# Optimization experiments

Hardware: AMD Instinct MI355X
Metric: run time of the kernel (lower is better)

Reference implementation:

```python
import jax, jax.numpy as jnp
import numpy as np

CONF_THRES = 0.1
IOU_THRES = 0.6
MAX_DET = 300
MAX_WH = 4096.0  # class offset for non-agnostic NMS
NEG_SLOPE = 0.01  # nn.LeakyReLU default


def xywh2xyxy(p):
    xy, wh = p[..., :2], p[..., 2:4]
    return jnp.concatenate([xy - wh / 2, xy + wh / 2], axis=-1)


def pairwise_iou(a, b):
    area_a = (a[:, 2] - a[:, 0]) * (a[:, 3] - a[:, 1])
    area_b = (b[:, 2] - b[:, 0]) * (b[:, 3] - b[:, 1])
    lt = jnp.maximum(a[:, None, :2], b[None, :, :2])
    rb = jnp.minimum(a[:, None, 2:], b[None, :, 2:])
    wh = jnp.clip(rb - lt, 0.0)
    inter = wh[..., 0] * wh[..., 1]
    return inter / (area_a[:, None] + area_b[None, :] - inter + 1e-7)


def nms_single(pred):  # pred: [N, 5+nc]
    boxes = xywh2xyxy(pred[:, :4])
    scores = pred[:, 5:] * pred[:, 4:5]  # obj * cls
    conf = jnp.max(scores, axis=1)
    cls = jnp.argmax(scores, axis=1)
    conf = jnp.where(conf > CONF_THRES, conf, 0.0)
    topv, topi = jax.lax.top_k(conf, MAX_DET)
    b = boxes[topi]                      # [K,4]
    c = cls[topi]
    valid = topv > CONF_THRES
    bo = b + (c.astype(b.dtype) * MAX_WH)[:, None]  # class-offset boxes
    iou = pairwise_iou(bo, bo)           # [K,K]
    idx = jnp.arange(MAX_DET)
    def body(i, keep):
        sup = keep[i] & (iou[i] > IOU_THRES) & (idx > i)
        return keep & ~sup
    keep = jax.lax.fori_loop(0, MAX_DET, body, valid)
    return b, keep


def bilinear_sample(feat, y, x):  # feat [C,H,W], y/x [K,P] -> [C,K,P]
    C, H, W = feat.shape
    y = jnp.clip(y, 0.0, H - 1.0)
    x = jnp.clip(x, 0.0, W - 1.0)
    y0 = jnp.floor(y).astype(jnp.int32)
    x0 = jnp.floor(x).astype(jnp.int32)
    y1 = jnp.minimum(y0 + 1, H - 1)
    x1 = jnp.minimum(x0 + 1, W - 1)
    ly = y - y0
    lx = x - x0
    return (feat[:, y0, x0] * ((1 - ly) * (1 - lx))
            + feat[:, y0, x1] * ((1 - ly) * lx)
            + feat[:, y1, x0] * (ly * (1 - lx))
            + feat[:, y1, x1] * (ly * lx))


def roi_align_1x1(feat, boxes, scale):  # feat [C,H,W], boxes [K,4] xyxy (input-px)
    b = boxes * scale
    w = jnp.maximum(b[:, 2] - b[:, 0], 1.0)
    h = jnp.maximum(b[:, 3] - b[:, 1], 1.0)
    off = jnp.array([0.5, 1.5], dtype=boxes.dtype)
    xs = b[:, 0:1] + off[None, :] * (w[:, None] / 2.0)  # [K,2]
    ys = b[:, 1:2] + off[None, :] * (h[:, None] / 2.0)
    yy = ys[:, jnp.array([0, 0, 1, 1])]  # [K,4] 2x2 grid
    xx = xs[:, jnp.array([0, 1, 0, 1])]
    v = bilinear_sample(feat, yy, xx)    # [C,K,4]
    return jnp.mean(v, axis=2).T         # [K,C]


def rescale_boxes(bbox, hw, hw0):  # scale_coords + normalize by orig shape
    gain = jnp.minimum(hw[0] / hw0[0], hw[1] / hw0[1])
    pad_x = (hw[1] - hw0[1] * gain) / 2.0
    pad_y = (hw[0] - hw0[0] * gain) / 2.0
    x1 = jnp.clip((bbox[:, 0] - pad_x) / gain, 0.0, hw0[1])
    y1 = jnp.clip((bbox[:, 1] - pad_y) / gain, 0.0, hw0[0])
    x2 = jnp.clip((bbox[:, 2] - pad_x) / gain, 0.0, hw0[1])
    y2 = jnp.clip((bbox[:, 3] - pad_y) / gain, 0.0, hw0[0])
    # divide by shapes[i][0] indexed [w,h,w,h]
    return jnp.stack([x1 / hw0[1], y1 / hw0[0], x2 / hw0[1], y2 / hw0[0]], axis=1)


def setup_inputs() -> dict:
    key = jax.random.key(0)
    ks = jax.random.split(key, 10)
    B, N, NC = 8, 25500, 80
    xy = jax.random.uniform(ks[0], (B, N, 2), minval=0.0, maxval=640.0)
    wh = jax.random.uniform(ks[1], (B, N, 2), minval=8.0, maxval=160.0)
    obj = jax.random.uniform(ks[2], (B, N, 1))
    cls = jax.random.uniform(ks[3], (B, N, NC))
    preds = jnp.concatenate([xy, wh, obj, cls], axis=-1)
    feat1 = jax.random.normal(ks[4], (B, 128, 80, 80), dtype=jnp.float32)
    feat2 = jax.random.normal(ks[5], (B, 256, 40, 40), dtype=jnp.float32)
    feat3 = jax.random.normal(ks[6], (B, 512, 20, 20), dtype=jnp.float32)
    feat4 = jax.random.normal(ks[7], (B, 1024, 10, 10), dtype=jnp.float32)
    orig_hw = jnp.tile(jnp.array([[720.0, 1280.0]], dtype=jnp.float32), (B, 1))
    W1 = jax.random.normal(ks[8], (1920, 256), dtype=jnp.float32) * 0.02
    b1 = jnp.zeros((256,), dtype=jnp.float32)
    W2 = jax.random.normal(ks[9], (256, 256), dtype=jnp.float32) * 0.02
    b2 = jnp.zeros((256,), dtype=jnp.float32)
    return {"preds": preds, "feat1": feat1, "feat2": feat2, "feat3": feat3,
            "feat4": feat4, "orig_hw": orig_hw, "W1": W1, "b1": b1,
            "W2": W2, "b2": b2}


def reference(preds, feat1, feat2, feat3, feat4, orig_hw, W1, b1, W2, b2):
    preds = jax.lax.stop_gradient(preds)  # out.detach() in the original
    hw = jnp.array(feat1.shape[-2:], dtype=preds.dtype) * 8.0  # network input h,w
    boxes, keep = jax.vmap(nms_single)(preds)  # [B,K,4], [B,K]
    f1 = jax.vmap(lambda f, b: roi_align_1x1(f, b, 1.0 / 8))(feat1, boxes)
    f2 = jax.vmap(lambda f, b: roi_align_1x1(f, b, 1.0 / 16))(feat2, boxes)
    f3 = jax.vmap(lambda f, b: roi_align_1x1(f, b, 1.0 / 32))(feat3, boxes)
    f4 = jax.vmap(lambda f, b: roi_align_1x1(f, b, 1.0 / 64))(feat4, boxes)
    f = jnp.concatenate([f1, f2, f3, f4], axis=-1)  # [B,K,1920]
    h = jax.nn.leaky_relu(f @ W1 + b1, NEG_SLOPE)
    h = jax.nn.leaky_relu(h @ W2 + b2, NEG_SLOPE)   # [B,K,256]
    bb = jax.vmap(lambda b, s: rescale_boxes(b, hw, s))(boxes, orig_hw)
    out = jnp.concatenate([bb, h], axis=-1)  # [B,K,260]
    return out * keep[..., None].astype(out.dtype)
```

## Files before the change

kernel.cpp:

```cpp
#include <hip/hip_runtime.h>
#include <hip/hip_bf16.h>
#include <cstdint>
#include <cstddef>

#define NBATCH 8
#define NANCH 25500
#define MAXDET 300
#define NBINS 2048
#define SCAT_BLKS 64

typedef __bf16 bf16x8 __attribute__((ext_vector_type(8)));
typedef float floatx4 __attribute__((ext_vector_type(4)));
typedef unsigned long long ull;

__device__ __forceinline__ int conf_bin(float v) {
  unsigned bits = __float_as_uint(v);
  int bin = (int)((bits - 0x3D800000u) >> 14);
  return bin > (NBINS - 1) ? (NBINS - 1) : bin;
}

#define CONF_TILE 64
__global__ __launch_bounds__(256) void conf_kernel(const float* __restrict__ preds,
                                                   float* __restrict__ conf,
                                                   int* __restrict__ cls,
                                                   int* __restrict__ zmem, int zints,
                                                   int total) {
  if (blockIdx.x < 33) {
    int base = blockIdx.x * 1024;
    #pragma unroll
    for (int k = 0; k < 4; ++k) {
      int i = base + k * 256 + threadIdx.x;
      if (i < zints) zmem[i] = 0;
    }
  }
  __shared__ float s[CONF_TILE * 85];
  int base = blockIdx.x * CONF_TILE;
  int nA = total - base; if (nA > CONF_TILE) nA = CONF_TILE;
  int n4 = (nA * 85) >> 2;
  const float4* g4 = (const float4*)(preds + (size_t)base * 85);
  float4* s4 = (float4*)s;
  for (int i = threadIdx.x; i < n4; i += 256) s4[i] = g4[i];
  __syncthreads();
  int lane16 = threadIdx.x & 15;
  int sub = threadIdx.x >> 4;
  #pragma unroll
  for (int r = 0; r < 4; ++r) {
    int a = r * 16 + sub;
    if (a < nA) {
      const float* row = s + a * 85;
      float obj = row[4];
      float best = -1.0f; int bc = 0;
      #pragma unroll
      for (int j = 0; j < 5; ++j) {
        int c = lane16 * 5 + j;
        float v = row[5 + c] * obj;
        if (v > best) { best = v; bc = c; }
      }
      #pragma unroll
      for (int m = 1; m < 16; m <<= 1) {
        float ov = __shfl_xor(best, m, 64);
        int   oc = __shfl_xor(bc,   m, 64);
        if (ov > best || (ov == best && oc < bc)) { best = ov; bc = oc; }
      }
      if (lane16 == 0) {
        int idx = base + a;
        conf[idx] = (best > 0.1f) ? best : 0.0f;
        cls[idx] = bc;
      }
    }
  }
}

struct TransArgs {
  const float* src[6];
  __hip_bfloat16* dst[6];
  int C[6], HW[6], tx[6], tpb[6], start[6];
};

__global__ __launch_bounds__(256) void trans_scatter_kernel(TransArgs a,
                                                            const float* __restrict__ conf,
                                                            const float* __restrict__ preds,
                                                            const int* __restrict__ clsg,
                                                            int* __restrict__ ghist,
                                                            int* __restrict__ gcnt,
                                                            int* __restrict__ ctr1,
                                                            float* __restrict__ gV,
                                                            int* __restrict__ gI,
                                                            float4* __restrict__ gBox) {
  #pragma clang fp contract(off)
  __shared__ __align__(16) char smem[8448];
  int bid = blockIdx.x;
  int t = threadIdx.y * 32 + threadIdx.x;

  if (bid < SCAT_BLKS) {
    int b = bid >> 3, seg = bid & 7;
    int* s_h = (int*)smem;
    int* shv = (int*)(smem + 8192);
    #pragma unroll
    for (int k = 0; k < 8; ++k) s_h[t + k * 256] = 0;
    if (t == 0) shv[0] = NBINS;
    __syncthreads();
    const int N4 = NANCH >> 2;
    int i0 = (N4 * seg) >> 3, i1 = (N4 * (seg + 1)) >> 3;
    const float4* cf4 = (const float4*)(conf + (size_t)b * NANCH);
    for (int i = i0 + t; i < i1; i += 256) {
      float4 v = cf4[i];
      if (v.x > 0.1f) atomicAdd(&s_h[conf_bin(v.x)], 1);
      if (v.y > 0.1f) atomicAdd(&s_h[conf_bin(v.y)], 1);
      if (v.z > 0.1f) atomicAdd(&s_h[conf_bin(v.z)], 1);
      if (v.w > 0.1f) atomicAdd(&s_h[conf_bin(v.w)], 1);
    }
    __syncthreads();
    #pragma unroll
    for (int k = 0; k < 8; ++k) {
      int bin = t + k * 256;
      int c = s_h[bin];
      if (c) atomicAdd(&ghist[b * NBINS + bin], c);
    }
    __syncthreads();
    if (t == 0) {
      __threadfence();
      atomicAdd(&ctr1[b], 1);
      while (atomicAdd(&ctr1[b], 0) < 8) __builtin_amdgcn_s_sleep(2);
      __threadfence();
    }
    __syncthreads();
    int r[8], suf[8], rs[8];
    int w = t >> 6, lane = t & 63;
    {
      #pragma unroll
      for (int k = 0; k < 8; ++k)
        r[k] = atomicAdd(&ghist[b * NBINS + (w * 8 + k) * 64 + lane], 0);
      int bsum = 0;
      #pragma unroll
      for (int k = 0; k < 8; ++k) {
        int s = r[k];
        #pragma unroll
        for (int d = 1; d < 64; d <<= 1) {
          int o = __shfl_down(s, d, 64);
          if (lane + d < 64) s += o;
        }
        suf[k] = s - r[k];
        rs[k] = __shfl(s, 0, 64);
        bsum += rs[k];
      }
      if (lane == 0) shv[4 + w] = bsum;
    }
    __syncthreads();
    {
      int p1 = shv[5], p2 = shv[6], p3 = shv[7];
      int total = shv[4] + p1 + p2 + p3;
      int target = total < 300 ? total : 300;
      int RS = (w == 0) ? (p1 + p2 + p3) : (w == 1) ? (p2 + p3) : (w == 2) ? p3 : 0;
      int run = RS;
      #pragma unroll
      for (int k = 7; k >= 0; --k) {
        int Sx = run + suf[k] + r[k];
        int Sx1 = Sx - r[k];
        int bin = (w * 8 + k) * 64 + lane;
        s_h[bin] = Sx1;
        if (total > 0 && Sx >= target && Sx1 < target) shv[0] = bin;
        run += rs[k];
      }
    }
    __syncthreads();
    int T = shv[0];
    for (int i = i0 + t; i < i1; i += 256) {
      float4 v4 = cf4[i];
      int ib = i * 4;
      float vv[4] = {v4.x, v4.y, v4.z, v4.w};
      #pragma unroll
      for (int q = 0; q < 4; ++q) {
        float v = vv[q];
        if (v > 0.1f) {
          int bin = conf_bin(v);
          if (bin >= T) {
            int slot = s_h[bin] + atomicAdd(&gcnt[b * NBINS + bin], 1);
            int idx = ib + q;
            const float* p = preds + ((size_t)b * NANCH + idx) * 85;
            float cx = p[0], cy = p[1], wq = p[2], hq = p[3];
            float hw2 = wq * 0.5f, hh2 = hq * 0.5f;
            float x1 = cx - hw2, y1 = cy - hh2, x2 = cx + hw2, y2 = cy + hh2;
            int c = clsg[(size_t)b * NANCH + idx];
            size_t g = (size_t)b * NANCH + slot;
            gV[g] = v;
            gI[g] = idx | (c << 20);
            gBox[g] = make_float4(x1, y1, x2, y2);
          }
        }
      }
    }
    return;
  }

  {
    float (*tile)[33] = (float(*)[33])smem;
    int bid2 = bid - SCAT_BLKS;
    int s = 0;
    #pragma unroll
    for (int i = 1; i < 6; ++i) if (bid2 >= a.start[i]) s = i;
    int local = bid2 - a.start[s];
    int C = a.C[s], HW = a.HW[s], tx0 = a.tx[s], tpb = a.tpb[s];
    int b = local / tpb;
    int rem = local - b * tpb;
    int p0 = (rem % tx0) * 32;
    int c0 = (rem / tx0) * 32;
    const float* inb = a.src[s] + (size_t)b * C * HW;
    __hip_bfloat16* outb = a.dst[s] + (size_t)b * C * HW;
    int tx = threadIdx.x, ty = threadIdx.y;
    #pragma unroll
    for (int k = 0; k < 32; k += 8) {
      int c = c0 + ty + k, p = p0 + tx;
      if (c < C && p < HW) tile[ty + k][tx] = inb[(size_t)c * HW + p];
    }
    __syncthreads();
    #pragma unroll
    for (int k = 0; k < 32; k += 8) {
      int p = p0 + ty + k, c = c0 + tx;
      if (p < HW && c < C) outb[(size_t)p * C + c] = __float2bfloat16(tile[tx][ty + k]);
    }
  }
}

__global__ __launch_bounds__(1024) void nms_kernel(const float* __restrict__ gV,
                                                   const int* __restrict__ gI,
                                                   const float4* __restrict__ gBox,
                                                   const int* __restrict__ ghist,
                                                   float* __restrict__ boxesWs, int* __restrict__ keepWs,
                                                   const float* __restrict__ orig_hw,
                                                   float* __restrict__ out) {
  #pragma clang fp contract(off)
  __shared__ __align__(16) char smem[30208];
  int*    s_h  = (int*)smem;
  float4* bo4  = (float4*)(smem + 8192);
  float (*bxx)[4] = (float(*)[4])(smem + 12992);
  ull   (*mask)[5] = (ull(*)[5])(smem + 17792);
  ull* keepw = (ull*)(smem + 29792);
  ull* nzrow = (ull*)(smem + 29832);
  int* shv   = (int*)(smem + 29872);
  int b = blockIdx.x;
  int t = threadIdx.x;

  if (t < 300) {
    bo4[t] = make_float4(0.0f, 0.0f, 0.0f, 0.0f);
    bxx[t][0] = 0.0f; bxx[t][1] = 0.0f; bxx[t][2] = 0.0f; bxx[t][3] = 0.0f;
  }
  if (t < 5) nzrow[t] = 0ULL;
  if (t == 0) { shv[0] = NBINS; shv[2] = 0; }
  {
    int r[8], suf[8], rs[8];
    int w = t >> 6, lane = t & 63;
    if (t < 256) {
      #pragma unroll
      for (int k = 0; k < 8; ++k)
        r[k] = ghist[b * NBINS + (w * 8 + k) * 64 + lane];
      int bsum = 0;
      #pragma unroll
      for (int k = 0; k < 8; ++k) {
        int s = r[k];
        #pragma unroll
        for (int d = 1; d < 64; d <<= 1) {
          int o = __shfl_down(s, d, 64);
          if (lane + d < 64) s += o;
        }
        suf[k] = s - r[k];
        rs[k] = __shfl(s, 0, 64);
        bsum += rs[k];
      }
      if (lane == 0) shv[4 + w] = bsum;
    }
    __syncthreads();
    if (t < 256) {
      int p1 = shv[5], p2 = shv[6], p3 = shv[7];
      int total = shv[4] + p1 + p2 + p3;
      int target = total < 300 ? total : 300;
      int RS = (w == 0) ? (p1 + p2 + p3) : (w == 1) ? (p2 + p3) : (w == 2) ? p3 : 0;
      int run = RS;
      #pragma unroll
      for (int k = 7; k >= 0; --k) {
        int Sx = run + suf[k] + r[k];
        int Sx1 = Sx - r[k];
        int bin = (w * 8 + k) * 64 + lane;
        s_h[bin] = Sx;
        if (total > 0 && Sx >= target && Sx1 < target) { shv[0] = bin; shv[2] = Sx; }
        run += rs[k];
      }
      if (t == 0) shv[1] = total;
    }
  }
  __syncthreads();
  int total = shv[1];
  int Kslots = shv[2];
  int nvalid = total < 300 ? total : 300;

  if (t >= nvalid && t < 300) {
    size_t bi = ((size_t)(b * 300 + t)) * 4;
    boxesWs[bi + 0] = 0.0f; boxesWs[bi + 1] = 0.0f;
    boxesWs[bi + 2] = 0.0f; boxesWs[bi + 3] = 0.0f;
  }
  if (t < 5) {
    int n = nvalid - t * 64;
    keepw[t] = (n <= 0) ? 0ULL : (n >= 64 ? ~0ULL : ((1ULL << n) - 1ULL));
  }

  {
    const float* vb = gV + (size_t)b * NANCH;
    const int*   ib2 = gI + (size_t)b * NANCH;
    for (int sIdx = t; sIdx < Kslots; sIdx += 1024) {
      float v = vb[sIdx];
      unsigned code = (unsigned)ib2[sIdx];
      int id = (int)(code & 0xFFFFFu);
      int bin = conf_bin(v);
      int lo = (bin + 1 < NBINS) ? s_h[bin + 1] : 0;
      int hi = s_h[bin];
      int rank = lo;
      for (int j = lo; j < hi; ++j) {
        float vj = vb[j];
        int ij = ib2[j] & 0xFFFFF;
        int gt = vj > v;
        int eq = (vj == v) & (ij < id);
        rank += gt | eq;
      }
      if (rank < 300) {
        float4 bx = gBox[(size_t)b * NANCH + sIdx];
        bxx[rank][0] = bx.x; bxx[rank][1] = bx.y; bxx[rank][2] = bx.z; bxx[rank][3] = bx.w;
        size_t bi = ((size_t)(b * 300 + rank)) * 4;
        boxesWs[bi + 0] = bx.x; boxesWs[bi + 1] = bx.y;
        boxesWs[bi + 2] = bx.z; boxesWs[bi + 3] = bx.w;
        int c = (int)(code >> 20);
        float off = (float)c * 4096.0f;
        float4 ob; ob.x = bx.x + off; ob.y = bx.y + off; ob.z = bx.z + off; ob.w = bx.w + off;
        bo4[rank] = ob;
      }
    }
  }
  __syncthreads();

  {
    int wv2 = t >> 6, ln = t & 63;
    if (wv2 < 10) {
      int w2 = wv2 >> 1, half = wv2 & 1;
      int j = w2 * 64 + ln;
      int jc = j < 300 ? j : 0;
      float4 jb = bo4[jc];
      float ja = (jb.z - jb.x) * (jb.w - jb.y);
      bool jv = j < 300;
      int iend = w2 * 64 + 64; if (iend > 300) iend = 300;
      int i0 = half * 150, i1 = i0 + 150; if (i1 > iend) i1 = iend;
      #pragma unroll 4
      for (int i = i0; i < i1; ++i) {
        float4 ib = bo4[i];
        float ai = (ib.z - ib.x) * (ib.w - ib.y);
        float ltx = fmaxf(ib.x, jb.x);
        float lty = fmaxf(ib.y, jb.y);
        float rbx = fminf(ib.z, jb.z);
        float rby = fminf(ib.w, jb.w);
        float wx = fmaxf(rbx - ltx, 0.0f);
        float wy = fmaxf(rby - lty, 0.0f);
        float inter = wx * wy;
        float iou = inter / (ai + ja - inter + 1e-7f);
        ull bal = __ballot(jv && (j > i) && (iou > 0.6f));
        if (ln == 0) {
          mask[i][w2] = bal;
          if (bal) atomicOr(&nzrow[i >> 6], 1ULL << (i & 63));
        }
      }
    }
  }
  __syncthreads();
  if (t == 0) {
    ull kw[5], nz[5];
    #pragma unroll
    for (int w2 = 0; w2 < 5; ++w2) { kw[w2] = keepw[w2]; nz[w2] = nzrow[w2]; }
    #pragma unroll
    for (int w2 = 0; w2 < 5; ++w2) {
      ull p = kw[w2] & nz[w2];
      while (p) {
        int l2 = __builtin_ctzll(p);
        p &= p - 1;
        int i = w2 * 64 + l2;
        for (int w3 = w2; w3 < 5; ++w3) {
          ull m = mask[i][w3];
          kw[w3] &= ~m;
          if (w3 == w2) p &= ~m;
        }
      }
    }
    #pragma unroll
    for (int w2 = 0; w2 < 5; ++w2) keepw[w2] = kw[w2];
  }
  __syncthreads();
  if (t < 300) {
    int kp = (int)((keepw[t >> 6] >> (t & 63)) & 1ULL);
    keepWs[b * 300 + t] = kp;
    float oh = orig_hw[b * 2 + 0], ow = orig_hw[b * 2 + 1];
    float gain = fminf(640.0f / oh, 640.0f / ow);
    float padx = (640.0f - ow * gain) * 0.5f;
    float pady = (640.0f - oh * gain) * 0.5f;
    float x1 = fminf(fmaxf((bxx[t][0] - padx) / gain, 0.0f), ow) / ow;
    float y1 = fminf(fmaxf((bxx[t][1] - pady) / gain, 0.0f), oh) / oh;
    float x2 = fminf(fmaxf((bxx[t][2] - padx) / gain, 0.0f), ow) / ow;
    float y2 = fminf(fmaxf((bxx[t][3] - pady) / gain, 0.0f), oh) / oh;
    size_t o = ((size_t)(b * 300 + t)) * 260;
    out[o + 0] = kp ? x1 : 0.0f;
    out[o + 1] = kp ? y1 : 0.0f;
    out[o + 2] = kp ? x2 : 0.0f;
    out[o + 3] = kp ? y2 : 0.0f;
  }
}

__global__ __launch_bounds__(256) void roi_kernel(const float* __restrict__ boxes,
                                                  const __hip_bfloat16* __restrict__ fT1, const __hip_bfloat16* __restrict__ fT2,
                                                  const __hip_bfloat16* __restrict__ fT3, const __hip_bfloat16* __restrict__ fT4,
                                                  __hip_bfloat16* __restrict__ f) {
  int b = blockIdx.x & 7;
  int r = blockIdx.x >> 3;
  __shared__ int t_off[4][16];
  __shared__ float t_w[4][16];
  int t = threadIdx.x;
  const int Hs[4] = {80, 40, 20, 10};
  const int Cs[4] = {128, 256, 512, 1024};
  const float ss[4] = {0.125f, 0.0625f, 0.03125f, 0.015625f};
  size_t bbase = ((size_t)(b * 300 + r)) * 4;
  float bx0 = boxes[bbase + 0];
  float by0 = boxes[bbase + 1];
  float bx1 = boxes[bbase + 2];
  float by1 = boxes[bbase + 3];
  if (t < 64) {
    int lv = t >> 4, k = t & 15, pp = k >> 2, nb = k & 3;
    float s = ss[lv];
    int H = Hs[lv], W = Hs[lv], C = Cs[lv];
    float b0 = bx0 * s, b1 = by0 * s, b2 = bx1 * s, b3 = by1 * s;
    float w = fmaxf(b2 - b0, 1.0f), h = fmaxf(b3 - b1, 1.0f);
    const float offv[2] = {0.5f, 1.5f};
    float px = b0 + offv[pp & 1] * (w * 0.5f);
    float py = b1 + offv[pp >> 1] * (h * 0.5f);
    float y = fminf(fmaxf(py, 0.0f), (float)(H - 1));
    float x = fminf(fmaxf(px, 0.0f), (float)(W - 1));
    int y0 = (int)floorf(y), x0 = (int)floorf(x);
    int y1 = min(y0 + 1, H - 1), x1 = min(x0 + 1, W - 1);
    float ly = y - (float)y0, lx = x - (float)x0;
    int yy = (nb & 2) ? y1 : y0;
    int xx = (nb & 1) ? x1 : x0;
    float wy = (nb & 2) ? ly : (1.0f - ly);
    float wx = (nb & 1) ? lx : (1.0f - lx);
    t_off[lv][k] = (yy * W + xx) * C;
    t_w[lv][k] = wy * wx;
  }
  __syncthreads();
  const __hip_bfloat16* bases[4] = {
    fT1 + (size_t)b * 6400 * 128,
    fT2 + (size_t)b * 1600 * 256,
    fT3 + (size_t)b * 400 * 512,
    fT4 + (size_t)b * 100 * 1024
  };
  __hip_bfloat16* frow = f + (size_t)(b * 300 + r) * 1920;
  int cbase = 0;
  #pragma unroll
  for (int lv = 0; lv < 4; ++lv) {
    int C = Cs[lv];
    const __hip_bfloat16* base = bases[lv];
    for (int c = t; c < C; c += 256) {
      float acc = 0.0f;
      #pragma unroll
      for (int k = 0; k < 16; ++k)
        acc += t_w[lv][k] * __bfloat162float(base[t_off[lv][k] + c]);
      frow[cbase + c] = __float2bfloat16(acc * 0.25f);
    }
    cbase += C;
  }
}

#define GLDS16(gp, lp) __builtin_amdgcn_global_load_lds( \
    (const __attribute__((address_space(1))) unsigned int*)(gp), \
    (__attribute__((address_space(3))) unsigned int*)(lp), 16, 0, 0)

__global__ __launch_bounds__(256) void gemm_tile_kernel(const __hip_bfloat16* __restrict__ A,
                                                        const __hip_bfloat16* __restrict__ BT,
                                                        const float* __restrict__ bias,
                                                        __hip_bfloat16* __restrict__ Cb,
                                                        float* __restrict__ Cf,
                                                        const int* __restrict__ keep,
                                                        int M, int N, int K, int ldc, int coff) {
  __shared__ __hip_bfloat16 sA[2][64 * 64];
  __shared__ __hip_bfloat16 sB[2][64 * 64];
  int tid = threadIdx.x;
  int bm = blockIdx.x * 64, bn = blockIdx.y * 64;
  int wave = tid >> 6, lane = tid & 63;
  int wr = wave >> 1, wc = wave & 1;
  int idx16 = lane & 15, kb = lane >> 4;
  floatx4 acc[2][2] = {};
  int nt = K >> 6;

  auto stage = [&](int buf, int t) {
    int k0 = t << 6;
    #pragma unroll
    for (int i = 0; i < 2; ++i) {
      int c = tid + i * 256;
      int row = c >> 3, cc = c & 7;
      int scc = cc ^ (row & 7);
      GLDS16(A + (size_t)(bm + row) * K + k0 + scc * 8,
             (char*)&sA[buf][0] + c * 16);
    }
    #pragma unroll
    for (int i = 0; i < 2; ++i) {
      int c = tid + i * 256;
      int row = c >> 3, cc = c & 7;
      int scc = cc ^ (row & 7);
      GLDS16(BT + (size_t)(bn + row) * K + k0 + scc * 8,
             (char*)&sB[buf][0] + c * 16);
    }
  };

  stage(0, 0);
  asm volatile("s_waitcnt vmcnt(0)" ::: "memory");
  __syncthreads();
  int cur = 0;
  for (int t = 0; t < nt; ++t) {
    if (t + 1 < nt) stage(cur ^ 1, t + 1);
    const char* Ab = (const char*)&sA[cur][0];
    const char* Bb = (const char*)&sB[cur][0];
    #pragma unroll
    for (int s = 0; s < 2; ++s) {
      bf16x8 af[2], bg[2];
      #pragma unroll
      for (int m = 0; m < 2; ++m) {
        int row = wr * 32 + m * 16 + idx16;
        int chunk = s * 4 + kb;
        af[m] = *(const bf16x8*)(Ab + row * 128 + ((chunk ^ (row & 7)) * 16));
      }
      #pragma unroll
      for (int n = 0; n < 2; ++n) {
        int row = wc * 32 + n * 16 + idx16;
        int chunk = s * 4 + kb;
        bg[n] = *(const bf16x8*)(Bb + row * 128 + ((chunk ^ (row & 7)) * 16));
      }
      #pragma unroll
      for (int m = 0; m < 2; ++m)
        #pragma unroll
        for (int n = 0; n < 2; ++n)
          acc[m][n] = __builtin_amdgcn_mfma_f32_16x16x32_bf16(af[m], bg[n], acc[m][n], 0, 0, 0);
    }
    asm volatile("s_waitcnt vmcnt(0)" ::: "memory");
    __syncthreads();
    cur ^= 1;
  }
  int col = lane & 15, rb4 = (lane >> 4) * 4;
  #pragma unroll
  for (int m = 0; m < 2; ++m) {
    #pragma unroll
    for (int n = 0; n < 2; ++n) {
      #pragma unroll
      for (int r = 0; r < 4; ++r) {
        int orow = bm + wr * 32 + m * 16 + rb4 + r;
        int ocol = bn + wc * 32 + n * 16 + col;
        if (orow >= M) continue;
        float v = acc[m][n][r] + bias[ocol];
        v = (v >= 0.0f) ? v : 0.01f * v;
        if (Cb) Cb[(size_t)orow * N + ocol] = __float2bfloat16(v);
        if (Cf) {
          float km = keep ? (keep[orow] ? 1.0f : 0.0f) : 1.0f;
          Cf[(size_t)orow * ldc + coff + ocol] = v * km;
        }
      }
    }
  }
}

extern "C" void kernel_launch(void* const* d_in, const int* in_sizes, int n_in,
                              void* d_out, int out_size, void* d_ws, size_t ws_size,
                              hipStream_t stream) {
  (void)in_sizes; (void)n_in; (void)out_size; (void)ws_size;
  const float* preds  = (const float*)d_in[0];
  const float* feat1  = (const float*)d_in[1];
  const float* feat2  = (const float*)d_in[2];
  const float* feat3  = (const float*)d_in[3];
  const float* feat4  = (const float*)d_in[4];
  const float* orighw = (const float*)d_in[5];
  const float* W1     = (const float*)d_in[6];
  const float* b1     = (const float*)d_in[7];
  const float* W2     = (const float*)d_in[8];
  const float* b2     = (const float*)d_in[9];
  float* out = (float*)d_out;

  char* ws = (char*)d_ws;
  size_t off = 0;
  auto alloc = [&](size_t bytes) -> void* {
    void* p = ws + off;
    off = (off + bytes + 255) & ~(size_t)255;
    return p;
  };
  const int BN = NBATCH * NANCH;
  float*  conf   = (float*)alloc((size_t)BN * 4);
  int*    cls    = (int*)  alloc((size_t)BN * 4);
  float*  gV     = (float*)alloc((size_t)BN * 4);
  int*    gI     = (int*)  alloc((size_t)BN * 4);
  float4* gBox   = (float4*)alloc((size_t)BN * 16);
  int*    ghist  = (int*)  alloc((size_t)NBATCH * NBINS * 4);
  int*    gcnt   = (int*)  alloc((size_t)NBATCH * NBINS * 4);
  int*    ctr1   = (int*)  alloc(256);
  const int zints = NBATCH * NBINS * 2 + 64;
  float*  boxes  = (float*)alloc((size_t)NBATCH * 300 * 4 * 4);
  int*    keep   = (int*)  alloc((size_t)NBATCH * 300 * 4);
  __hip_bfloat16* fT1  = (__hip_bfloat16*)alloc((size_t)NBATCH * 6400 * 128 * 2);
  __hip_bfloat16* fT2  = (__hip_bfloat16*)alloc((size_t)NBATCH * 1600 * 256 * 2);
  __hip_bfloat16* fT3  = (__hip_bfloat16*)alloc((size_t)NBATCH * 400 * 512 * 2);
  __hip_bfloat16* fT4  = (__hip_bfloat16*)alloc((size_t)NBATCH * 100 * 1024 * 2);
  __hip_bfloat16* fmat = (__hip_bfloat16*)alloc((size_t)2400 * 1920 * 2);
  __hip_bfloat16* h1b  = (__hip_bfloat16*)alloc((size_t)2400 * 256 * 2);
  __hip_bfloat16* W1T  = (__hip_bfloat16*)alloc((size_t)256 * 1920 * 2);
  __hip_bfloat16* W2T  = (__hip_bfloat16*)alloc((size_t)256 * 256 * 2);

  conf_kernel<<<(BN + CONF_TILE - 1) / CONF_TILE, 256, 0, stream>>>(preds, conf, cls,
                                                                    ghist, zints, BN);

  TransArgs ta;
  ta.src[0] = feat1; ta.dst[0] = fT1; ta.C[0] = 128;  ta.HW[0] = 6400; ta.tx[0] = 200;
  ta.src[1] = feat2; ta.dst[1] = fT2; ta.C[1] = 256;  ta.HW[1] = 1600; ta.tx[1] = 50;
  ta.src[2] = feat3; ta.dst[2] = fT3; ta.C[2] = 512;  ta.HW[2] = 400;  ta.tx[2] = 13;
  ta.src[3] = feat4; ta.dst[3] = fT4; ta.C[3] = 1024; ta.HW[3] = 100;  ta.tx[3] = 4;
  ta.src[4] = W1;    ta.dst[4] = W1T; ta.C[4] = 1920; ta.HW[4] = 256;  ta.tx[4] = 8;
  ta.src[5] = W2;    ta.dst[5] = W2T; ta.C[5] = 256;  ta.HW[5] = 256;  ta.tx[5] = 8;
  int n_tiles = 0;
  for (int s = 0; s < 6; ++s) {
    int ty = (ta.C[s] + 31) / 32;
    int nbatch = (s < 4) ? NBATCH : 1;
    ta.tpb[s] = ta.tx[s] * ty;
    ta.start[s] = n_tiles;
    n_tiles += ta.tpb[s] * nbatch;
  }
  trans_scatter_kernel<<<SCAT_BLKS + n_tiles, dim3(32, 8), 0, stream>>>(ta, conf, preds, cls,
                                                                        ghist, gcnt, ctr1,
                                                                        gV, gI, gBox);

  nms_kernel<<<NBATCH, 1024, 0, stream>>>(gV, gI, gBox, ghist, boxes, keep, orighw, out);

  roi_kernel<<<2400, 256, 0, stream>>>(boxes, fT1, fT2, fT3, fT4, fmat);
  gemm_tile_kernel<<<dim3(38, 4), 256, 0, stream>>>(fmat, W1T, b1, h1b, nullptr, nullptr,
                                                    2400, 256, 1920, 0, 0);
  gemm_tile_kernel<<<dim3(38, 4), 256, 0, stream>>>(h1b, W2T, b2, nullptr, out, keep,
                                                    2400, 256, 256, 260, 4);
}
```

Measured before the change: 133.3 us.

## Overlap feature transpose with NMS and widen transpose tiles to 64x64

Splits the histogram/scatter work into its own kernel and fuses the feature-map/weight transpose into the NMS kernel, so the 8 serial NMS blocks run alongside the transpose blocks instead of leaving the GPU mostly idle. The transpose now uses 64x64 tiles with float4 loads and 16-byte bf16 stores, four tiles per 1024-thread block. The cost is an extra kernel launch and a larger shared-memory footprint (66 KB) that may limit occupancy. The layout also assumes C is a multiple of 64.

```diff
diff --git a/kernel.cpp b/kernel.cpp
--- a/kernel.cpp
+++ b/kernel.cpp
@@ -12,6 +12,8 @@
 typedef __bf16 bf16x8 __attribute__((ext_vector_type(8)));
 typedef float floatx4 __attribute__((ext_vector_type(4)));
 typedef unsigned long long ull;
+
+struct __align__(16) bfvec8 { __hip_bfloat16 h[8]; };
 
 __device__ __forceinline__ int conf_bin(float v) {
   unsigned bits = __float_as_uint(v);
@@ -71,166 +73,199 @@
   }
 }
 
+__global__ __launch_bounds__(256) void scatter_kernel(const float* __restrict__ conf,
+                                                      const float* __restrict__ preds,
+                                                      const int* __restrict__ clsg,
+                                                      int* __restrict__ ghist,
+                                                      int* __restrict__ gcnt,
+                                                      int* __restrict__ ctr1,
+                                                      float* __restrict__ gV,
+                                                      int* __restrict__ gI,
+                                                      float4* __restrict__ gBox) {
+  #pragma clang fp contract(off)
+  __shared__ __align__(16) char smem[8448];
+  int bid = blockIdx.x;
+  int t = threadIdx.x;
+  int b = bid >> 3, seg = bid & 7;
+  int* s_h = (int*)smem;
+  int* shv = (int*)(smem + 8192);
+  #pragma unroll
+  for (int k = 0; k < 8; ++k) s_h[t + k * 256] = 0;
+  if (t == 0) shv[0] = NBINS;
+  __syncthreads();
+  const int N4 = NANCH >> 2;
+  int i0 = (N4 * seg) >> 3, i1 = (N4 * (seg + 1)) >> 3;
+  const float4* cf4 = (const float4*)(conf + (size_t)b * NANCH);
+  for (int i = i0 + t; i < i1; i += 256) {
+    float4 v = cf4[i];
+    if (v.x > 0.1f) atomicAdd(&s_h[conf_bin(v.x)], 1);
+    if (v.y > 0.1f) atomicAdd(&s_h[conf_bin(v.y)], 1);
+    if (v.z > 0.1f) atomicAdd(&s_h[conf_bin(v.z)], 1);
+    if (v.w > 0.1f) atomicAdd(&s_h[conf_bin(v.w)], 1);
+  }
+  __syncthreads();
+  #pragma unroll
+  for (int k = 0; k < 8; ++k) {
+    int bin = t + k * 256;
+    int c = s_h[bin];
+    if (c) atomicAdd(&ghist[b * NBINS + bin], c);
+  }
+  __syncthreads();
+  if (t == 0) {
+    __threadfence();
+    atomicAdd(&ctr1[b], 1);
+    while (atomicAdd(&ctr1[b], 0) < 8) __builtin_amdgcn_s_sleep(2);
+    __threadfence();
+  }
+  __syncthreads();
+  int r[8], suf[8], rs[8];
+  int w = t >> 6, lane = t & 63;
+  {
+    #pragma unroll
+    for (int k = 0; k < 8; ++k)
+      r[k] = atomicAdd(&ghist[b * NBINS + (w * 8 + k) * 64 + lane], 0);
+    int bsum = 0;
+    #pragma unroll
+    for (int k = 0; k < 8; ++k) {
+      int s = r[k];
+      #pragma unroll
+      for (int d = 1; d < 64; d <<= 1) {
+        int o = __shfl_down(s, d, 64);
+        if (lane + d < 64) s += o;
+      }
+      suf[k] = s - r[k];
+      rs[k] = __shfl(s, 0, 64);
+      bsum += rs[k];
+    }
+    if (lane == 0) shv[4 + w] = bsum;
+  }
+  __syncthreads();
+  {
+    int p1 = shv[5], p2 = shv[6], p3 = shv[7];
+    int total = shv[4] + p1 + p2 + p3;
+    int target = total < 300 ? total : 300;
+    int RS = (w == 0) ? (p1 + p2 + p3) : (w == 1) ? (p2 + p3) : (w == 2) ? p3 : 0;
+    int run = RS;
+    #pragma unroll
+    for (int k = 7; k >= 0; --k) {
+      int Sx = run + suf[k] + r[k];
+      int Sx1 = Sx - r[k];
+      int bin = (w * 8 + k) * 64 + lane;
+      s_h[bin] = Sx1;
+      if (total > 0 && Sx >= target && Sx1 < target) shv[0] = bin;
+      run += rs[k];
+    }
+  }
+  __syncthreads();
+  int T = shv[0];
+  for (int i = i0 + t; i < i1; i += 256) {
+    float4 v4 = cf4[i];
+    int ib = i * 4;
+    float vv[4] = {v4.x, v4.y, v4.z, v4.w};
+    #pragma unroll
+    for (int q = 0; q < 4; ++q) {
+      float v = vv[q];
+      if (v > 0.1f) {
+        int bin = conf_bin(v);
+        if (bin >= T) {
+          int slot = s_h[bin] + atomicAdd(&gcnt[b * NBINS + bin], 1);
+          int idx = ib + q;
+          const float* p = preds + ((size_t)b * NANCH + idx) * 85;
+          float cx = p[0], cy = p[1], wq = p[2], hq = p[3];
+          float hw2 = wq * 0.5f, hh2 = hq * 0.5f;
+          float x1 = cx - hw2, y1 = cy - hh2, x2 = cx + hw2, y2 = cy + hh2;
+          int c = clsg[(size_t)b * NANCH + idx];
+          size_t g = (size_t)b * NANCH + slot;
+          gV[g] = v;
+          gI[g] = idx | (c << 20);
+          gBox[g] = make_float4(x1, y1, x2, y2);
+        }
+      }
+    }
+  }
+}
+
 struct TransArgs {
   const float* src[6];
   __hip_bfloat16* dst[6];
   int C[6], HW[6], tx[6], tpb[6], start[6];
 };
 
-__global__ __launch_bounds__(256) void trans_scatter_kernel(TransArgs a,
-                                                            const float* __restrict__ conf,
-                                                            const float* __restrict__ preds,
-                                                            const int* __restrict__ clsg,
-                                                            int* __restrict__ ghist,
-                                                            int* __restrict__ gcnt,
-                                                            int* __restrict__ ctr1,
-                                                            float* __restrict__ gV,
-                                                            int* __restrict__ gI,
-                                                            float4* __restrict__ gBox) {
+__global__ __launch_bounds__(1024) void nms_trans_kernel(TransArgs a,
+                                                         const float* __restrict__ gV,
+                                                         const int* __restrict__ gI,
+                                                         const float4* __restrict__ gBox,
+                                                         const int* __restrict__ ghist,
+                                                         float* __restrict__ boxesWs, int* __restrict__ keepWs,
+                                                         const float* __restrict__ orig_hw,
+                                                         float* __restrict__ out,
+                                                         int n_trans_tiles) {
   #pragma clang fp contract(off)
-  __shared__ __align__(16) char smem[8448];
+  __shared__ __align__(16) char smem[66560];
   int bid = blockIdx.x;
-  int t = threadIdx.y * 32 + threadIdx.x;
-
-  if (bid < SCAT_BLKS) {
-    int b = bid >> 3, seg = bid & 7;
-    int* s_h = (int*)smem;
-    int* shv = (int*)(smem + 8192);
-    #pragma unroll
-    for (int k = 0; k < 8; ++k) s_h[t + k * 256] = 0;
-    if (t == 0) shv[0] = NBINS;
+  int t = threadIdx.x;
+
+  if (bid >= 8) {
+    int g = t >> 8, lt = t & 255;
+    int gt = (bid - 8) * 4 + g;
+    float (*tile)[65] = (float(*)[65])(smem + g * 16640);
+    bool act = gt < n_trans_tiles;
+    int C = 0, HW = 0, p0 = 0, c0 = 0;
+    const float* inb = nullptr;
+    __hip_bfloat16* outb = nullptr;
+    if (act) {
+      int s = 0;
+      #pragma unroll
+      for (int i = 1; i < 6; ++i) if (gt >= a.start[i]) s = i;
+      int local = gt - a.start[s];
+      C = a.C[s]; HW = a.HW[s];
+      int txp = a.tx[s], tpb = a.tpb[s];
+      int b = local / tpb;
+      int rem = local - b * tpb;
+      p0 = (rem % txp) * 64;
+      c0 = (rem / txp) * 64;
+      inb = a.src[s] + (size_t)b * C * HW;
+      outb = a.dst[s] + (size_t)b * C * HW;
+      int rgrp = lt >> 4, cg = lt & 15;
+      if (p0 + 64 <= HW) {
+        #pragma unroll
+        for (int k = 0; k < 4; ++k) {
+          int r = k * 16 + rgrp;
+          float4 v = *(const float4*)(inb + (size_t)(c0 + r) * HW + p0 + cg * 4);
+          tile[r][cg * 4 + 0] = v.x; tile[r][cg * 4 + 1] = v.y;
+          tile[r][cg * 4 + 2] = v.z; tile[r][cg * 4 + 3] = v.w;
+        }
+      } else {
+        int nvp = HW - p0;
+        #pragma unroll
+        for (int k = 0; k < 4; ++k) {
+          int r = k * 16 + rgrp;
+          const float* src = inb + (size_t)(c0 + r) * HW + p0;
+          #pragma unroll
+          for (int j = 0; j < 4; ++j) {
+            int pp = cg * 4 + j;
+            tile[r][pp] = (pp < nvp) ? src[pp] : 0.0f;
+          }
+        }
+      }
+    }
     __syncthreads();
-    const int N4 = NANCH >> 2;
-    int i0 = (N4 * seg) >> 3, i1 = (N4 * (seg + 1)) >> 3;
-    const float4* cf4 = (const float4*)(conf + (size_t)b * NANCH);
-    for (int i = i0 + t; i < i1; i += 256) {
-      float4 v = cf4[i];
-      if (v.x > 0.1f) atomicAdd(&s_h[conf_bin(v.x)], 1);
-      if (v.y > 0.1f) atomicAdd(&s_h[conf_bin(v.y)], 1);
-      if (v.z > 0.1f) atomicAdd(&s_h[conf_bin(v.z)], 1);
-      if (v.w > 0.1f) atomicAdd(&s_h[conf_bin(v.w)], 1);
-    }
-    __syncthreads();
-    #pragma unroll
-    for (int k = 0; k < 8; ++k) {
-      int bin = t + k * 256;
-      int c = s_h[bin];
-      if (c) atomicAdd(&ghist[b * NBINS + bin], c);
-    }
-    __syncthreads();
-    if (t == 0) {
-      __threadfence();
-      atomicAdd(&ctr1[b], 1);
-      while (atomicAdd(&ctr1[b], 0) < 8) __builtin_amdgcn_s_sleep(2);
-      __threadfence();
-    }
-    __syncthreads();
-    int r[8], suf[8], rs[8];
-    int w = t >> 6, lane = t & 63;
-    {
-      #pragma unroll
-      for (int k = 0; k < 8; ++k)
-        r[k] = atomicAdd(&ghist[b * NBINS + (w * 8 + k) * 64 + lane], 0);
-      int bsum = 0;
-      #pragma unroll
-      for (int k = 0; k < 8; ++k) {
-        int s = r[k];
-        #pragma unroll
-        for (int d = 1; d < 64; d <<= 1) {
-          int o = __shfl_down(s, d, 64);
-          if (lane + d < 64) s += o;
-        }
-        suf[k] = s - r[k];
-        rs[k] = __shfl(s, 0, 64);
-        bsum += rs[k];
-      }
-      if (lane == 0) shv[4 + w] = bsum;
-    }
-    __syncthreads();
-    {
-      int p1 = shv[5], p2 = shv[6], p3 = shv[7];
-      int total = shv[4] + p1 + p2 + p3;
-      int target = total < 300 ? total : 300;
-      int RS = (w == 0) ? (p1 + p2 + p3) : (w == 1) ? (p2 + p3) : (w == 2) ? p3 : 0;
-      int run = RS;
-      #pragma unroll
-      for (int k = 7; k >= 0; --k) {
-        int Sx = run + suf[k] + r[k];
-        int Sx1 = Sx - r[k];
-        int bin = (w * 8 + k) * 64 + lane;
-        s_h[bin] = Sx1;
-        if (total > 0 && Sx >= target && Sx1 < target) shv[0] = bin;
-        run += rs[k];
-      }
-    }
-    __syncthreads();
-    int T = shv[0];
-    for (int i = i0 + t; i < i1; i += 256) {
-      float4 v4 = cf4[i];
-      int ib = i * 4;
-      float vv[4] = {v4.x, v4.y, v4.z, v4.w};
-      #pragma unroll
-      for (int q = 0; q < 4; ++q) {
-        float v = vv[q];
-        if (v > 0.1f) {
-          int bin = conf_bin(v);
-          if (bin >= T) {
-            int slot = s_h[bin] + atomicAdd(&gcnt[b * NBINS + bin], 1);
-            int idx = ib + q;
-            const float* p = preds + ((size_t)b * NANCH + idx) * 85;
-            float cx = p[0], cy = p[1], wq = p[2], hq = p[3];
-            float hw2 = wq * 0.5f, hh2 = hq * 0.5f;
-            float x1 = cx - hw2, y1 = cy - hh2, x2 = cx + hw2, y2 = cy + hh2;
-            int c = clsg[(size_t)b * NANCH + idx];
-            size_t g = (size_t)b * NANCH + slot;
-            gV[g] = v;
-            gI[g] = idx | (c << 20);
-            gBox[g] = make_float4(x1, y1, x2, y2);
-          }
+    if (act) {
+      int cb = (lt & 7) * 8;
+      #pragma unroll
+      for (int pass = 0; pass < 2; ++pass) {
+        int p = pass * 32 + (lt >> 3);
+        if (p0 + p < HW) {
+          bfvec8 o;
+          #pragma unroll
+          for (int j = 0; j < 8; ++j) o.h[j] = __float2bfloat16(tile[cb + j][p]);
+          *(bfvec8*)(outb + (size_t)(p0 + p) * C + c0 + cb) = o;
         }
       }
     }
     return;
   }
 
-  {
-    float (*tile)[33] = (float(*)[33])smem;
-    int bid2 = bid - SCAT_BLKS;
-    int s = 0;
-    #pragma unroll
-    for (int i = 1; i < 6; ++i) if (bid2 >= a.start[i]) s = i;
-    int local = bid2 - a.start[s];
-    int C = a.C[s], HW = a.HW[s], tx0 = a.tx[s], tpb = a.tpb[s];
-    int b = local / tpb;
-    int rem = local - b * tpb;
-    int p0 = (rem % tx0) * 32;
-    int c0 = (rem / tx0) * 32;
-    const float* inb = a.src[s] + (size_t)b * C * HW;
-    __hip_bfloat16* outb = a.dst[s] + (size_t)b * C * HW;
-    int tx = threadIdx.x, ty = threadIdx.y;
-    #pragma unroll
-    for (int k = 0; k < 32; k += 8) {
-      int c = c0 + ty + k, p = p0 + tx;
-      if (c < C && p < HW) tile[ty + k][tx] = inb[(size_t)c * HW + p];
-    }
-    __syncthreads();
-    #pragma unroll
-    for (int k = 0; k < 32; k += 8) {
-      int p = p0 + ty + k, c = c0 + tx;
-      if (p < HW && c < C) outb[(size_t)p * C + c] = __float2bfloat16(tile[tx][ty + k]);
-    }
-  }
-}
-
-__global__ __launch_bounds__(1024) void nms_kernel(const float* __restrict__ gV,
-                                                   const int* __restrict__ gI,
-                                                   const float4* __restrict__ gBox,
-                                                   const int* __restrict__ ghist,
-                                                   float* __restrict__ boxesWs, int* __restrict__ keepWs,
-                                                   const float* __restrict__ orig_hw,
-                                                   float* __restrict__ out) {
-  #pragma clang fp contract(off)
-  __shared__ __align__(16) char smem[30208];
   int*    s_h  = (int*)smem;
   float4* bo4  = (float4*)(smem + 8192);
   float (*bxx)[4] = (float(*)[4])(smem + 12992);
@@ -238,8 +273,7 @@
   ull* keepw = (ull*)(smem + 29792);
   ull* nzrow = (ull*)(smem + 29832);
   int* shv   = (int*)(smem + 29872);
-  int b = blockIdx.x;
-  int t = threadIdx.x;
+  int b = bid;
 
   if (t < 300) {
     bo4[t] = make_float4(0.0f, 0.0f, 0.0f, 0.0f);
@@ -614,26 +648,29 @@
   conf_kernel<<<(BN + CONF_TILE - 1) / CONF_TILE, 256, 0, stream>>>(preds, conf, cls,
                                                                     ghist, zints, BN);
 
+  scatter_kernel<<<SCAT_BLKS, 256, 0, stream>>>(conf, preds, cls, ghist, gcnt, ctr1,
+                                                gV, gI, gBox);
+
   TransArgs ta;
-  ta.src[0] = feat1; ta.dst[0] = fT1; ta.C[0] = 128;  ta.HW[0] = 6400; ta.tx[0] = 200;
-  ta.src[1] = feat2; ta.dst[1] = fT2; ta.C[1] = 256;  ta.HW[1] = 1600; ta.tx[1] = 50;
-  ta.src[2] = feat3; ta.dst[2] = fT3; ta.C[2] = 512;  ta.HW[2] = 400;  ta.tx[2] = 13;
-  ta.src[3] = feat4; ta.dst[3] = fT4; ta.C[3] = 1024; ta.HW[3] = 100;  ta.tx[3] = 4;
-  ta.src[4] = W1;    ta.dst[4] = W1T; ta.C[4] = 1920; ta.HW[4] = 256;  ta.tx[4] = 8;
-  ta.src[5] = W2;    ta.dst[5] = W2T; ta.C[5] = 256;  ta.HW[5] = 256;  ta.tx[5] = 8;
+  ta.src[0] = feat1; ta.dst[0] = fT1; ta.C[0] = 128;  ta.HW[0] = 6400;
+  ta.src[1] = feat2; ta.dst[1] = fT2; ta.C[1] = 256;  ta.HW[1] = 1600;
+  ta.src[2] = feat3; ta.dst[2] = fT3; ta.C[2] = 512;  ta.HW[2] = 400;
+  ta.src[3] = feat4; ta.dst[3] = fT4; ta.C[3] = 1024; ta.HW[3] = 100;
+  ta.src[4] = W1;    ta.dst[4] = W1T; ta.C[4] = 1920; ta.HW[4] = 256;
+  ta.src[5] = W2;    ta.dst[5] = W2T; ta.C[5] = 256;  ta.HW[5] = 256;
   int n_tiles = 0;
   for (int s = 0; s < 6; ++s) {
-    int ty = (ta.C[s] + 31) / 32;
+    int txp = (ta.HW[s] + 63) / 64;
+    int tyc = ta.C[s] / 64;
     int nbatch = (s < 4) ? NBATCH : 1;
-    ta.tpb[s] = ta.tx[s] * ty;
+    ta.tx[s] = txp;
+    ta.tpb[s] = txp * tyc;
     ta.start[s] = n_tiles;
     n_tiles += ta.tpb[s] * nbatch;
   }
-  trans_scatter_kernel<<<SCAT_BLKS + n_tiles, dim3(32, 8), 0, stream>>>(ta, conf, preds, cls,
-                                                                        ghist, gcnt, ctr1,
-                                                                        gV, gI, gBox);
-
-  nms_kernel<<<NBATCH, 1024, 0, stream>>>(gV, gI, gBox, ghist, boxes, keep, orighw, out);
+  nms_trans_kernel<<<8 + (n_tiles + 3) / 4, 1024, 0, stream>>>(ta, gV, gI, gBox, ghist,
+                                                               boxes, keep, orighw, out,
+                                                               n_tiles);
 
   roi_kernel<<<2400, 256, 0, stream>>>(boxes, fT1, fT2, fT3, fT4, fmat);
   gemm_tile_kernel<<<dim3(38, 4), 256, 0, stream>>>(fmat, W1T, b1, h1b, nullptr, nullptr,
```

Result: faster. 129.7 us (-2.7%).
